# Kernel tuning notes

Measured on AMD Instinct MI355X. Metric: run time of the kernel, lower is better.

The kernel has to match this reference:

```python
import jax, jax.numpy as jnp
import numpy as np

GROUPS = 8
HEADS = 4
EPS = 1e-5


def setup_inputs() -> dict:
    key = jax.random.key(0)
    ks = jax.random.split(key, 5)
    b, c, h, w = 4, 256, 64, 64
    x = jax.random.normal(ks[0], (b, c, h, w), dtype=jnp.float32)
    gn_w = jnp.ones((c,), dtype=jnp.float32)
    gn_b = jnp.zeros((c,), dtype=jnp.float32)
    qkv_w = jax.random.normal(ks[1], (3 * c, c), dtype=jnp.float32) * (c ** -0.5)
    qkv_b = jax.random.normal(ks[2], (3 * c,), dtype=jnp.float32) * 0.01
    proj_w = jax.random.normal(ks[3], (c, c), dtype=jnp.float32) * (c ** -0.5)
    proj_b = jax.random.normal(ks[4], (c,), dtype=jnp.float32) * 0.01
    return {"x": x, "gn_w": gn_w, "gn_b": gn_b, "qkv_w": qkv_w,
            "qkv_b": qkv_b, "proj_w": proj_w, "proj_b": proj_b}


def reference(x, gn_w, gn_b, qkv_w, qkv_b, proj_w, proj_b):
    b, c, h, w = x.shape
    head_dim = c // HEADS
    n = h * w

    # GroupNorm (biased variance, per torch)
    xg = x.reshape(b, GROUPS, c // GROUPS, h, w)
    mean = xg.mean(axis=(2, 3, 4), keepdims=True)
    var = xg.var(axis=(2, 3, 4), keepdims=True)
    xn = ((xg - mean) * jax.lax.rsqrt(var + EPS)).reshape(b, c, h, w)
    xn = xn * gn_w[None, :, None, None] + gn_b[None, :, None, None]

    # 1x1 conv qkv: [b,3c,h,w]
    qkv = jnp.einsum('oc,bchw->bohw', qkv_w, xn) + qkv_b[None, :, None, None]
    # split channel dim as (3, heads, head_dim), flatten spatial -> [b,3,H,d,n]
    qkv = qkv.reshape(b, 3, HEADS, head_dim, n)
    q, k, v = qkv[:, 0], qkv[:, 1], qkv[:, 2]  # each [b,H,d,n]

    scale = head_dim ** -0.5
    attn = jnp.einsum('bhci,bhcj->bhij', q, k) * scale  # [b,H,n,n]
    attn = jax.nn.softmax(attn, axis=-1)
    out = jnp.einsum('bhij,bhcj->bhci', attn, v)  # [b,H,d,n]
    out = out.reshape(b, c, h, w)

    out = jnp.einsum('oc,bchw->bohw', proj_w, out) + proj_b[None, :, None, None]
    return out + x
```

## Files before the change

### kernel.cpp

```cpp
#include <hip/hip_runtime.h>
#include <math.h>

#define NPIX 4096
#define CCH 256

typedef __attribute__((ext_vector_type(4))) float f32x4;
typedef __attribute__((ext_vector_type(16))) float f32x16;
typedef __attribute__((ext_vector_type(8))) short s16x8;
typedef unsigned short u16;

__device__ __forceinline__ short bf16_rne(float x) {
  union { float f; unsigned u; } c; c.f = x;
  unsigned r = c.u + 0x7FFF + ((c.u >> 16) & 1);
  return (short)(r >> 16);
}
__device__ __forceinline__ unsigned cvtpk2(float lo, float hi) {
  unsigned r;
  asm("v_cvt_pk_bf16_f32 %0, %1, %2" : "=v"(r) : "v"(lo), "v"(hi));
  return r;
}
__device__ __forceinline__ unsigned pack2(float a, float b) {
  return cvtpk2(a, b);
}
__device__ __forceinline__ float max3f(float a, float b, float c) {
  float d;
  asm("v_max3_f32 %0, %1, %2, %3" : "=v"(d) : "v"(a), "v"(b), "v"(c));
  return d;
}
__device__ __forceinline__ float bf16_to_f32(unsigned short v) {
  return __uint_as_float(((unsigned)v) << 16);
}

__device__ __forceinline__ void plane32_swap(unsigned& a, unsigned& b) {
#if __has_builtin(__builtin_amdgcn_permlane32_swap)
  auto r = __builtin_amdgcn_permlane32_swap(a, b, false, false);
  a = r[0]; b = r[1];
#else
  asm("s_nop 2\n\tv_permlane32_swap_b32 %0, %1\n\ts_nop 2" : "+v"(a), "+v"(b));
#endif
}
__device__ __forceinline__ float red_max_half(float x) {
  unsigned a = __float_as_uint(x), b = a;
  plane32_swap(a, b);
  return fmaxf(__uint_as_float(a), __uint_as_float(b));
}
__device__ __forceinline__ float red_sum_half(float x) {
  unsigned a = __float_as_uint(x), b = a;
  plane32_swap(a, b);
  return __uint_as_float(a) + __uint_as_float(b);
}

#define QSCALE 0.18033688011f

__global__ __launch_bounds__(256) void gn_stats_wcvt(
    const float* __restrict__ x, const float* __restrict__ qkv_w, const float* __restrict__ proj_w,
    const float* __restrict__ qkv_b, double2* __restrict__ partials,
    u16* __restrict__ wq, u16* __restrict__ wp, float* __restrict__ biasq)
{
  const int blk = blockIdx.x, tid = threadIdx.x;
#pragma unroll
  for (int p = 0; p < 4; ++p) {
    int idx = blk * 1024 + p * 256 + tid;
    if (idx < 196608) {
      float v = qkv_w[idx];
      if (idx < 65536) v *= QSCALE;
      wq[idx] = (u16)bf16_rne(v);
    } else {
      int j = idx - 196608;
      wp[j] = (u16)bf16_rne(proj_w[j]);
    }
    if (idx < 768) {
      float bv = qkv_b[idx];
      if (idx < 256) bv *= QSCALE;
      biasq[idx] = bv;
    }
  }
  const int bg = blk >> 3, chunk = blk & 7;
  const float4* base = (const float4*)(x + (size_t)bg * 131072 + (size_t)chunk * 16384);
  double s = 0.0, ss = 0.0;
  for (int idx = tid; idx < 4096; idx += 256) {
    float4 v = base[idx];
    s  += (double)v.x + (double)v.y + (double)v.z + (double)v.w;
    ss += (double)v.x * v.x + (double)v.y * v.y + (double)v.z * v.z + (double)v.w * v.w;
  }
  __shared__ double rs[256], rss[256];
  rs[tid] = s; rss[tid] = ss;
  __syncthreads();
  for (int off = 128; off > 0; off >>= 1) {
    if (tid < off) { rs[tid] += rs[tid + off]; rss[tid] += rss[tid + off]; }
    __syncthreads();
  }
  if (tid == 0) {
    double2 p; p.x = rs[0]; p.y = rss[0];
    partials[blk] = p;
  }
}

__global__ __launch_bounds__(256) void gn_apply_t2(
    const float* __restrict__ x, const double2* __restrict__ partials,
    const float* __restrict__ gn_w, const float* __restrict__ gn_b,
    u16* __restrict__ Xt)
{
  const int b = blockIdx.z, c0 = blockIdx.y * 64, n0 = blockIdx.x * 64;
  const int tid = threadIdx.x;
  __shared__ u16 T[64 * 68];
  __shared__ float sal[64], sbe[64], smv[2], srv[2];
  if (tid < 2) {
    int bg = b * 8 + (c0 >> 5) + tid;
    double s = 0.0, ss = 0.0;
    for (int c = 0; c < 8; ++c) { double2 p = partials[bg * 8 + c]; s += p.x; ss += p.y; }
    double mean = s / 131072.0;
    double var  = ss / 131072.0 - mean * mean;
    smv[tid] = (float)mean;
    srv[tid] = (float)(1.0 / sqrt(var + 1e-5));
  }
  __syncthreads();
  if (tid < 64) {
    int g = tid >> 5;
    int ch = c0 + tid;
    float a = srv[g] * gn_w[ch];
    sal[tid] = a;
    sbe[tid] = gn_b[ch] - smv[g] * a;
  }
  __syncthreads();
  const int n4 = (tid & 15) * 4, cr = tid >> 4;
#pragma unroll
  for (int p = 0; p < 4; ++p) {
    int cl = cr + 16 * p;
    int c = c0 + cl;
    float a = sal[cl], bt = sbe[cl];
    float4 v = *(const float4*)&x[((size_t)b * CCH + c) * NPIX + n0 + n4];
    T[(n4 + 0) * 68 + cl] = (u16)bf16_rne(v.x * a + bt);
    T[(n4 + 1) * 68 + cl] = (u16)bf16_rne(v.y * a + bt);
    T[(n4 + 2) * 68 + cl] = (u16)bf16_rne(v.z * a + bt);
    T[(n4 + 3) * 68 + cl] = (u16)bf16_rne(v.w * a + bt);
  }
  __syncthreads();
#pragma unroll
  for (int it = 0; it < 2; ++it) {
    int linear = it * 256 + tid;
    int n = linear >> 3, ch = linear & 7;
    s16x8 v = *(const s16x8*)&T[n * 68 + ch * 8];
    *(s16x8*)&Xt[((size_t)b * NPIX + n0 + n) * CCH + c0 + ch * 8] = v;
  }
}

__global__ __launch_bounds__(256) void qkv_gemm_kernel(
    const u16* __restrict__ Wbf, const float* __restrict__ biasv, const u16* __restrict__ Xt,
    u16* __restrict__ Qt, u16* __restrict__ Kt, u16* __restrict__ Vb)
{
  const int nblk = blockIdx.x, m0 = blockIdx.y * 64;
  const int tid = threadIdx.x, wave = tid >> 6, lane = tid & 63;
  const int n16 = lane & 15, quad = lane >> 4;
  const int n0 = nblk * 128 + wave * 32;

  f32x4 acc[4][2];
#pragma unroll
  for (int a = 0; a < 4; ++a)
#pragma unroll
    for (int c = 0; c < 2; ++c) acc[a][c] = (f32x4){0.f, 0.f, 0.f, 0.f};

#pragma unroll
  for (int k0 = 0; k0 < 256; k0 += 32) {
    s16x8 af[4], bfr[2];
#pragma unroll
    for (int msub = 0; msub < 4; ++msub)
      af[msub] = *(const s16x8*)&Wbf[(size_t)(m0 + msub * 16 + n16) * 256 + k0 + quad * 8];
#pragma unroll
    for (int nsub = 0; nsub < 2; ++nsub)
      bfr[nsub] = *(const s16x8*)&Xt[(size_t)(n0 + nsub * 16 + n16) * 256 + k0 + quad * 8];
#pragma unroll
    for (int msub = 0; msub < 4; ++msub)
#pragma unroll
      for (int nsub = 0; nsub < 2; ++nsub)
        acc[msub][nsub] = __builtin_amdgcn_mfma_f32_16x16x32_bf16(af[msub], bfr[nsub], acc[msub][nsub], 0, 0, 0);
  }

  __shared__ u16 T[8704];
  if (m0 < 512) {
#pragma unroll
    for (int msub = 0; msub < 4; ++msub)
#pragma unroll
      for (int nsub = 0; nsub < 2; ++nsub) {
        float b0 = biasv[m0 + msub * 16 + quad * 4 + 0];
        float b1 = biasv[m0 + msub * 16 + quad * 4 + 1];
        float b2 = biasv[m0 + msub * 16 + quad * 4 + 2];
        float b3 = biasv[m0 + msub * 16 + quad * 4 + 3];
        uint2 w2;
        w2.x = pack2(acc[msub][nsub][0] + b0, acc[msub][nsub][1] + b1);
        w2.y = pack2(acc[msub][nsub][2] + b2, acc[msub][nsub][3] + b3);
        *(uint2*)&T[(wave * 32 + nsub * 16 + n16) * 68 + msub * 16 + quad * 4] = w2;
      }
    __syncthreads();
    u16* dst = (m0 < 256) ? Qt : Kt;
    const int coff = m0 & 255;
#pragma unroll
    for (int it = 0; it < 4; ++it) {
      int linear = it * 256 + tid;
      int n = linear >> 3, ch = linear & 7;
      s16x8 v = *(const s16x8*)&T[n * 68 + ch * 8];
      *(s16x8*)&dst[(size_t)(nblk * 128 + n) * 256 + coff + ch * 8] = v;
    }
  } else {
#pragma unroll
    for (int msub = 0; msub < 4; ++msub)
#pragma unroll
      for (int nsub = 0; nsub < 2; ++nsub) {
        int ncol = wave * 32 + nsub * 16 + n16;
#pragma unroll
        for (int r = 0; r < 4; ++r) {
          int m = msub * 16 + quad * 4 + r;
          T[m * 136 + ncol] = (u16)bf16_rne(acc[msub][nsub][r] + biasv[m0 + m]);
        }
      }
    __syncthreads();
    const int b = (nblk * 128) >> 12, i0n = (nblk * 128) & 4095;
#pragma unroll
    for (int it = 0; it < 4; ++it) {
      int linear = it * 256 + tid;
      int mloc = linear >> 4, ch = linear & 15;
      s16x8 v = *(const s16x8*)&T[mloc * 136 + ch * 8];
      int c = (m0 - 512) + mloc;
      *(s16x8*)&Vb[((size_t)b * CCH + c) * NPIX + i0n + ch * 8] = v;
    }
  }
}

__device__ __forceinline__ void kv_load6(
    const u16* __restrict__ Kb, const u16* __restrict__ Vg, int h, int j0, int sj, int part,
    s16x8& k0, s16x8& k1, s16x8& v0, s16x8& v1)
{
  const s16x8* kp = (const s16x8*)&Kb[(size_t)(j0 + sj) * 256 + h * 64 + part * 16];
  const s16x8* vp = (const s16x8*)&Vg[(size_t)sj * NPIX + j0 + part * 16];
  k0 = kp[0]; k1 = kp[1]; v0 = vp[0]; v1 = vp[1];
}
__device__ __forceinline__ void kv_store6(
    u16* Ksb, u16* Vsb, int sbase,
    s16x8 k0, s16x8 k1, s16x8 v0, s16x8 v1)
{
  *(s16x8*)&Ksb[sbase]       = k0;
  *(s16x8*)&Ksb[sbase + 256] = k1;
  *(s16x8*)&Vsb[sbase]       = v0;
  *(s16x8*)&Vsb[sbase + 256] = v1;
}

__device__ __forceinline__ void attn_tile6(
    const u16* Ksb, const u16* Vsb, const s16x8 qf[4], int lane,
    f32x16 ot[2], float& m_i, float& l_i)
{
  f32x16 st[2];
#pragma unroll
  for (int r = 0; r < 16; ++r) { st[0][r] = 0.f; st[1][r] = 0.f; }

  __builtin_amdgcn_s_setprio(1);
#pragma unroll
  for (int kq = 0; kq < 4; ++kq)
#pragma unroll
    for (int jsub = 0; jsub < 2; ++jsub) {
      s16x8 a = *(const s16x8*)&Ksb[(jsub * 4 + kq) * 512 + lane * 8];
      st[jsub] = __builtin_amdgcn_mfma_f32_32x32x16_bf16(a, qf[kq], st[jsub], 0, 0, 0);
    }
  __builtin_amdgcn_s_setprio(0);

  float c0 = max3f(st[0][0],  st[0][1],  st[0][2]);
  float c1 = max3f(st[0][3],  st[0][4],  st[0][5]);
  float c2 = max3f(st[0][6],  st[0][7],  st[0][8]);
  float c3 = max3f(st[0][9],  st[0][10], st[0][11]);
  float c4 = max3f(st[0][12], st[0][13], st[0][14]);
  float c5 = max3f(st[0][15], st[1][0],  st[1][1]);
  float c6 = max3f(st[1][2],  st[1][3],  st[1][4]);
  float c7 = max3f(st[1][5],  st[1][6],  st[1][7]);
  float c8 = max3f(st[1][8],  st[1][9],  st[1][10]);
  float c9 = max3f(st[1][11], st[1][12], st[1][13]);
  float d0 = max3f(c0, c1, c2);
  float d1 = max3f(c3, c4, c5);
  float d2 = max3f(c6, c7, c8);
  float d3 = max3f(c9, st[1][14], st[1][15]);
  float tm = fmaxf(fmaxf(d0, d1), fmaxf(d2, d3));
  tm = red_max_half(tm);

  if (__any(tm > m_i + 8.0f)) {
    float mn = fmaxf(m_i, tm);
    float al = __builtin_amdgcn_exp2f(m_i - mn);
    m_i = mn;
    l_i *= al;
#pragma unroll
    for (int r = 0; r < 16; ++r) { ot[0][r] *= al; ot[1][r] *= al; }
  }

#pragma unroll
  for (int f = 0; f < 2; ++f)
#pragma unroll
    for (int r = 0; r < 16; ++r)
      st[f][r] = __builtin_amdgcn_exp2f(st[f][r] - m_i);

  float s0 = (st[0][0] + st[0][1]) + (st[0][2]  + st[0][3]);
  float s1 = (st[0][4] + st[0][5]) + (st[0][6]  + st[0][7]);
  float s2 = (st[0][8] + st[0][9]) + (st[0][10] + st[0][11]);
  float s3 = (st[0][12]+ st[0][13])+ (st[0][14] + st[0][15]);
  float s4 = (st[1][0] + st[1][1]) + (st[1][2]  + st[1][3]);
  float s5 = (st[1][4] + st[1][5]) + (st[1][6]  + st[1][7]);
  float s6 = (st[1][8] + st[1][9]) + (st[1][10] + st[1][11]);
  float s7 = (st[1][12]+ st[1][13])+ (st[1][14] + st[1][15]);
  float ps = ((s0 + s1) + (s2 + s3)) + ((s4 + s5) + (s6 + s7));
  ps = red_sum_half(ps);
  l_i += ps;

#pragma unroll
  for (int jq = 0; jq < 4; ++jq) {
    const int jsub = jq >> 1;
    const int b0 = (jq & 1) * 8;
    const int b1 = b0 + 4;
    unsigned u0 = cvtpk2(st[jsub][b0 + 0], st[jsub][b0 + 1]);
    unsigned u1 = cvtpk2(st[jsub][b0 + 2], st[jsub][b0 + 3]);
    unsigned u2 = cvtpk2(st[jsub][b1 + 0], st[jsub][b1 + 1]);
    unsigned u3 = cvtpk2(st[jsub][b1 + 2], st[jsub][b1 + 3]);
    plane32_swap(u0, u2);
    plane32_swap(u1, u3);
    union { unsigned u[4]; s16x8 v; } pu;
    pu.u[0] = u0; pu.u[1] = u1; pu.u[2] = u2; pu.u[3] = u3;
    __builtin_amdgcn_s_setprio(1);
#pragma unroll
    for (int dsub = 0; dsub < 2; ++dsub) {
      s16x8 a = *(const s16x8*)&Vsb[(dsub * 4 + jq) * 512 + lane * 8];
      ot[dsub] = __builtin_amdgcn_mfma_f32_32x32x16_bf16(a, pu.v, ot[dsub], 0, 0, 0);
    }
    __builtin_amdgcn_s_setprio(0);
  }
}

__global__ __launch_bounds__(256, 4) void attn_kernel6(
    const u16* __restrict__ Qt, const u16* __restrict__ Kt,
    const u16* __restrict__ Vb, u16* __restrict__ P0, u16* __restrict__ P1,
    float* __restrict__ mlbuf)
{
  const int b = blockIdx.z, h = blockIdx.y;
  const int xb = blockIdx.x;
  const int half = xb >> 5, iblk = xb & 31;
  const int tid = threadIdx.x;
  const int wave = tid >> 6, lane = tid & 63;
  const int i0w = iblk * 128 + wave * 32;

  __shared__ u16 Ks[2][4096];
  __shared__ u16 Vs[2][4096];

  const u16* Qb = Qt + (size_t)b * NPIX * 256;
  const u16* Kb = Kt + (size_t)b * NPIX * 256;
  const u16* Vg = Vb + ((size_t)b * CCH + h * 64) * NPIX;

  s16x8 qf[4];
#pragma unroll
  for (int kq = 0; kq < 4; ++kq)
    qf[kq] = *(const s16x8*)&Qb[(size_t)(i0w + (lane & 31)) * 256 + h * 64 + kq * 16 + (lane >> 5) * 8];

  f32x16 ot[2];
#pragma unroll
  for (int r = 0; r < 16; ++r) { ot[0][r] = 0.f; ot[1][r] = 0.f; }
  float m_i = -1e30f;
  float l_i = 0.f;

  const int sj = tid >> 2;
  const int part = tid & 3;
  const int sbase = ((sj >> 5) * 4 + part) * 512 + (sj & 31) * 8;
  const int jbase = half * 2048;

  s16x8 k0, k1, v0, v1;

  kv_load6(Kb, Vg, h, jbase, sj, part, k0, k1, v0, v1);
  kv_store6(Ks[0], Vs[0], sbase, k0, k1, v0, v1);
  __syncthreads();

#pragma unroll 1
  for (int t = 0; t < 30; t += 2) {
    kv_load6(Kb, Vg, h, jbase + (t + 1) * 64, sj, part, k0, k1, v0, v1);
    attn_tile6(Ks[0], Vs[0], qf, lane, ot, m_i, l_i);
    kv_store6(Ks[1], Vs[1], sbase, k0, k1, v0, v1);
    __syncthreads();
    kv_load6(Kb, Vg, h, jbase + (t + 2) * 64, sj, part, k0, k1, v0, v1);
    attn_tile6(Ks[1], Vs[1], qf, lane, ot, m_i, l_i);
    kv_store6(Ks[0], Vs[0], sbase, k0, k1, v0, v1);
    __syncthreads();
  }
  kv_load6(Kb, Vg, h, jbase + 31 * 64, sj, part, k0, k1, v0, v1);
  attn_tile6(Ks[0], Vs[0], qf, lane, ot, m_i, l_i);
  kv_store6(Ks[1], Vs[1], sbase, k0, k1, v0, v1);
  __syncthreads();
  attn_tile6(Ks[1], Vs[1], qf, lane, ot, m_i, l_i);

  float rl = 1.0f / l_i;
  u16* dst = (half == 0) ? P0 : P1;
  const size_t rowbase = (size_t)((size_t)b * NPIX + i0w + (lane & 31)) * 256 + h * 64 + (lane >> 5) * 4;
#pragma unroll
  for (int dsub = 0; dsub < 2; ++dsub)
#pragma unroll
    for (int q = 0; q < 4; ++q) {
      uint2 w2;
      w2.x = cvtpk2(ot[dsub][4 * q + 0] * rl, ot[dsub][4 * q + 1] * rl);
      w2.y = cvtpk2(ot[dsub][4 * q + 2] * rl, ot[dsub][4 * q + 3] * rl);
      *(uint2*)&dst[rowbase + dsub * 32 + q * 8] = w2;
    }
  if (lane < 32) {
    int idx = half * 65536 + b * 16384 + h * 4096 + i0w + lane;
    float2 ml; ml.x = m_i; ml.y = l_i;
    *(float2*)&mlbuf[idx * 2] = ml;
  }
}

__global__ __launch_bounds__(256) void proj_gemm_cmb(
    const u16* __restrict__ Wp, const float* __restrict__ proj_b,
    const u16* __restrict__ P0, const u16* __restrict__ P1, const float* __restrict__ mlbuf,
    const float* __restrict__ x, float* __restrict__ out)
{
  const int nblk = blockIdx.x, m0 = blockIdx.y * 64;
  const int tid = threadIdx.x, wave = tid >> 6, lane = tid & 63;
  const int n16 = lane & 15, quad = lane >> 4;
  const int n0 = nblk * 128 + wave * 32;

  float w0h[2][4], w1h[2][4];
#pragma unroll
  for (int ns = 0; ns < 2; ++ns) {
    int row = n0 + ns * 16 + n16;
    int bb = row >> 12, ii = row & 4095;
#pragma unroll
    for (int h = 0; h < 4; ++h) {
      int idx = bb * 16384 + h * 4096 + ii;
      float2 ml0 = *(const float2*)&mlbuf[(size_t)idx * 2];
      float2 ml1 = *(const float2*)&mlbuf[(size_t)(65536 + idx) * 2];
      float m = fmaxf(ml0.x, ml1.x);
      float cc0 = ml0.y * __builtin_amdgcn_exp2f(ml0.x - m);
      float cc1 = ml1.y * __builtin_amdgcn_exp2f(ml1.x - m);
      float rn = 1.0f / (cc0 + cc1);
      w0h[ns][h] = cc0 * rn;
      w1h[ns][h] = cc1 * rn;
    }
  }

  f32x4 acc[4][2];
#pragma unroll
  for (int a = 0; a < 4; ++a)
#pragma unroll
    for (int c = 0; c < 2; ++c) acc[a][c] = (f32x4){0.f, 0.f, 0.f, 0.f};

#pragma unroll
  for (int k0 = 0; k0 < 256; k0 += 32) {
    const int h = k0 >> 6;
    s16x8 af[4], bfr[2];
#pragma unroll
    for (int msub = 0; msub < 4; ++msub)
      af[msub] = *(const s16x8*)&Wp[(size_t)(m0 + msub * 16 + n16) * 256 + k0 + quad * 8];
#pragma unroll
    for (int nsub = 0; nsub < 2; ++nsub) {
      int row = n0 + nsub * 16 + n16;
      size_t off = (size_t)row * 256 + k0 + quad * 8;
      s16x8 a = *(const s16x8*)&P0[off];
      s16x8 c = *(const s16x8*)&P1[off];
      float w0 = w0h[nsub][h], w1 = w1h[nsub][h];
      union { unsigned u[4]; s16x8 v; } o;
#pragma unroll
      for (int e = 0; e < 4; ++e) {
        float lo = w0 * bf16_to_f32((unsigned short)a[2 * e])     + w1 * bf16_to_f32((unsigned short)c[2 * e]);
        float hi = w0 * bf16_to_f32((unsigned short)a[2 * e + 1]) + w1 * bf16_to_f32((unsigned short)c[2 * e + 1]);
        o.u[e] = cvtpk2(lo, hi);
      }
      bfr[nsub] = o.v;
    }
#pragma unroll
    for (int msub = 0; msub < 4; ++msub)
#pragma unroll
      for (int nsub = 0; nsub < 2; ++nsub)
        acc[msub][nsub] = __builtin_amdgcn_mfma_f32_16x16x32_bf16(af[msub], bfr[nsub], acc[msub][nsub], 0, 0, 0);
  }

  __shared__ float T[64 * 132];
#pragma unroll
  for (int msub = 0; msub < 4; ++msub)
#pragma unroll
    for (int nsub = 0; nsub < 2; ++nsub) {
      int ncol = wave * 32 + nsub * 16 + n16;
#pragma unroll
      for (int r = 0; r < 4; ++r) {
        int m = msub * 16 + quad * 4 + r;
        T[m * 132 + ncol] = acc[msub][nsub][r];
      }
    }
  __syncthreads();
  const int b = (nblk * 128) >> 12, i0n = (nblk * 128) & 4095;
#pragma unroll
  for (int it = 0; it < 8; ++it) {
    int linear = it * 256 + tid;
    int m = linear >> 5, ch = linear & 31;
    f32x4 v = *(const f32x4*)&T[m * 132 + ch * 4];
    float bs = proj_b[m0 + m];
    size_t g = ((size_t)b * CCH + m0 + m) * NPIX + i0n + ch * 4;
    float4 rv = *(const float4*)&x[g];
    float4 o;
    o.x = v[0] + bs + rv.x; o.y = v[1] + bs + rv.y;
    o.z = v[2] + bs + rv.z; o.w = v[3] + bs + rv.w;
    *(float4*)&out[g] = o;
  }
}

extern "C" void kernel_launch(void* const* d_in, const int* in_sizes, int n_in,
                              void* d_out, int out_size, void* d_ws, size_t ws_size,
                              hipStream_t stream)
{
  const float* x      = (const float*)d_in[0];
  const float* gn_w   = (const float*)d_in[1];
  const float* gn_b   = (const float*)d_in[2];
  const float* qkv_w  = (const float*)d_in[3];
  const float* qkv_b  = (const float*)d_in[4];
  const float* proj_w = (const float*)d_in[5];
  const float* proj_b = (const float*)d_in[6];
  float* out = (float*)d_out;

  float* ws    = (float*)d_ws;
  float* biasq = ws + 2048;
  double2* partials = (double2*)(ws + 2816);
  u16*   wq    = (u16*)(ws + 4096);
  u16*   wp    = (u16*)(ws + 102400);
  u16*   Xt    = (u16*)(ws + 135168);
  u16*   Qt    = (u16*)(ws + 2232320);
  u16*   Kt    = (u16*)(ws + 4329472);
  u16*   Vb    = (u16*)(ws + 6426624);
  u16*   Ot    = (u16*)(ws + 8523776);
  float* mlbuf = ws + 10620928;

  u16* P0 = Xt;

  gn_stats_wcvt<<<256, 256, 0, stream>>>(x, qkv_w, proj_w, qkv_b, partials, wq, wp, biasq);
  gn_apply_t2<<<dim3(64, 4, 4), 256, 0, stream>>>(x, partials, gn_w, gn_b, Xt);
  qkv_gemm_kernel<<<dim3(128, 12), 256, 0, stream>>>(wq, biasq, Xt, Qt, Kt, Vb);
  attn_kernel6<<<dim3(64, 4, 4), 256, 0, stream>>>(Qt, Kt, Vb, P0, Ot, mlbuf);
  proj_gemm_cmb<<<dim3(128, 4), 256, 0, stream>>>(wp, proj_b, P0, Ot, mlbuf, x, out);
}
```

Baseline: 240.1 us.

## Load attention K/V fragments directly from global memory, removing LDS staging

The attention kernel no longer stages K and V tiles in double-buffered shared memory with block barriers. Each wave now reads its MFMA operand fragments for K and V directly from global memory into registers, once per 64-key tile. This removes the LDS writes, LDS reads and __syncthreads, but each of the four waves in a block now fetches the same K/V data separately. That raises L2/global traffic and exposes load latency without explicit prefetch.

```diff
diff --git a/kernel.cpp b/kernel.cpp
--- a/kernel.cpp
+++ b/kernel.cpp
@@ -226,28 +226,17 @@
   }
 }
 
-__device__ __forceinline__ void kv_load6(
-    const u16* __restrict__ Kb, const u16* __restrict__ Vg, int h, int j0, int sj, int part,
-    s16x8& k0, s16x8& k1, s16x8& v0, s16x8& v1)
-{
-  const s16x8* kp = (const s16x8*)&Kb[(size_t)(j0 + sj) * 256 + h * 64 + part * 16];
-  const s16x8* vp = (const s16x8*)&Vg[(size_t)sj * NPIX + j0 + part * 16];
-  k0 = kp[0]; k1 = kp[1]; v0 = vp[0]; v1 = vp[1];
-}
-__device__ __forceinline__ void kv_store6(
-    u16* Ksb, u16* Vsb, int sbase,
-    s16x8 k0, s16x8 k1, s16x8 v0, s16x8 v1)
-{
-  *(s16x8*)&Ksb[sbase]       = k0;
-  *(s16x8*)&Ksb[sbase + 256] = k1;
-  *(s16x8*)&Vsb[sbase]       = v0;
-  *(s16x8*)&Vsb[sbase + 256] = v1;
-}
-
-__device__ __forceinline__ void attn_tile6(
-    const u16* Ksb, const u16* Vsb, const s16x8 qf[4], int lane,
+__device__ __forceinline__ void attn_tile7(
+    const u16* kt, const u16* vt, const s16x8 qf[4],
     f32x16 ot[2], float& m_i, float& l_i)
 {
+  s16x8 kf[8];
+#pragma unroll
+  for (int jsub = 0; jsub < 2; ++jsub)
+#pragma unroll
+    for (int kq = 0; kq < 4; ++kq)
+      kf[jsub * 4 + kq] = *(const s16x8*)(kt + jsub * 32 * 256 + kq * 16);
+
   f32x16 st[2];
 #pragma unroll
   for (int r = 0; r < 16; ++r) { st[0][r] = 0.f; st[1][r] = 0.f; }
@@ -256,11 +245,16 @@
 #pragma unroll
   for (int kq = 0; kq < 4; ++kq)
 #pragma unroll
-    for (int jsub = 0; jsub < 2; ++jsub) {
-      s16x8 a = *(const s16x8*)&Ksb[(jsub * 4 + kq) * 512 + lane * 8];
-      st[jsub] = __builtin_amdgcn_mfma_f32_32x32x16_bf16(a, qf[kq], st[jsub], 0, 0, 0);
-    }
+    for (int jsub = 0; jsub < 2; ++jsub)
+      st[jsub] = __builtin_amdgcn_mfma_f32_32x32x16_bf16(kf[jsub * 4 + kq], qf[kq], st[jsub], 0, 0, 0);
   __builtin_amdgcn_s_setprio(0);
+
+  s16x8 vf[8];
+#pragma unroll
+  for (int dsub = 0; dsub < 2; ++dsub)
+#pragma unroll
+    for (int jq = 0; jq < 4; ++jq)
+      vf[dsub * 4 + jq] = *(const s16x8*)(vt + dsub * 32 * NPIX + jq * 16);
 
   float c0 = max3f(st[0][0],  st[0][1],  st[0][2]);
   float c1 = max3f(st[0][3],  st[0][4],  st[0][5]);
@@ -321,15 +315,13 @@
     pu.u[0] = u0; pu.u[1] = u1; pu.u[2] = u2; pu.u[3] = u3;
     __builtin_amdgcn_s_setprio(1);
 #pragma unroll
-    for (int dsub = 0; dsub < 2; ++dsub) {
-      s16x8 a = *(const s16x8*)&Vsb[(dsub * 4 + jq) * 512 + lane * 8];
-      ot[dsub] = __builtin_amdgcn_mfma_f32_32x32x16_bf16(a, pu.v, ot[dsub], 0, 0, 0);
-    }
+    for (int dsub = 0; dsub < 2; ++dsub)
+      ot[dsub] = __builtin_amdgcn_mfma_f32_32x32x16_bf16(vf[dsub * 4 + jq], pu.v, ot[dsub], 0, 0, 0);
     __builtin_amdgcn_s_setprio(0);
   }
 }
 
-__global__ __launch_bounds__(256, 4) void attn_kernel6(
+__global__ __launch_bounds__(256, 4) void attn_kernel7(
     const u16* __restrict__ Qt, const u16* __restrict__ Kt,
     const u16* __restrict__ Vb, u16* __restrict__ P0, u16* __restrict__ P1,
     float* __restrict__ mlbuf)
@@ -341,17 +333,16 @@
   const int wave = tid >> 6, lane = tid & 63;
   const int i0w = iblk * 128 + wave * 32;
 
-  __shared__ u16 Ks[2][4096];
-  __shared__ u16 Vs[2][4096];
-
   const u16* Qb = Qt + (size_t)b * NPIX * 256;
   const u16* Kb = Kt + (size_t)b * NPIX * 256;
   const u16* Vg = Vb + ((size_t)b * CCH + h * 64) * NPIX;
 
+  const int l31 = lane & 31, lh8 = (lane >> 5) * 8;
+
   s16x8 qf[4];
 #pragma unroll
   for (int kq = 0; kq < 4; ++kq)
-    qf[kq] = *(const s16x8*)&Qb[(size_t)(i0w + (lane & 31)) * 256 + h * 64 + kq * 16 + (lane >> 5) * 8];
+    qf[kq] = *(const s16x8*)&Qb[(size_t)(i0w + l31) * 256 + h * 64 + kq * 16 + lh8];
 
   f32x16 ot[2];
 #pragma unroll
@@ -359,37 +350,17 @@
   float m_i = -1e30f;
   float l_i = 0.f;
 
-  const int sj = tid >> 2;
-  const int part = tid & 3;
-  const int sbase = ((sj >> 5) * 4 + part) * 512 + (sj & 31) * 8;
-  const int jbase = half * 2048;
-
-  s16x8 k0, k1, v0, v1;
-
-  kv_load6(Kb, Vg, h, jbase, sj, part, k0, k1, v0, v1);
-  kv_store6(Ks[0], Vs[0], sbase, k0, k1, v0, v1);
-  __syncthreads();
+  const u16* kbase = Kb + (size_t)(half * 2048 + l31) * 256 + h * 64 + lh8;
+  const u16* vbase = Vg + (size_t)l31 * NPIX + half * 2048 + lh8;
 
 #pragma unroll 1
-  for (int t = 0; t < 30; t += 2) {
-    kv_load6(Kb, Vg, h, jbase + (t + 1) * 64, sj, part, k0, k1, v0, v1);
-    attn_tile6(Ks[0], Vs[0], qf, lane, ot, m_i, l_i);
-    kv_store6(Ks[1], Vs[1], sbase, k0, k1, v0, v1);
-    __syncthreads();
-    kv_load6(Kb, Vg, h, jbase + (t + 2) * 64, sj, part, k0, k1, v0, v1);
-    attn_tile6(Ks[1], Vs[1], qf, lane, ot, m_i, l_i);
-    kv_store6(Ks[0], Vs[0], sbase, k0, k1, v0, v1);
-    __syncthreads();
-  }
-  kv_load6(Kb, Vg, h, jbase + 31 * 64, sj, part, k0, k1, v0, v1);
-  attn_tile6(Ks[0], Vs[0], qf, lane, ot, m_i, l_i);
-  kv_store6(Ks[1], Vs[1], sbase, k0, k1, v0, v1);
-  __syncthreads();
-  attn_tile6(Ks[1], Vs[1], qf, lane, ot, m_i, l_i);
+  for (int t = 0; t < 32; ++t) {
+    attn_tile7(kbase + (size_t)t * 64 * 256, vbase + t * 64, qf, ot, m_i, l_i);
+  }
 
   float rl = 1.0f / l_i;
   u16* dst = (half == 0) ? P0 : P1;
-  const size_t rowbase = (size_t)((size_t)b * NPIX + i0w + (lane & 31)) * 256 + h * 64 + (lane >> 5) * 4;
+  const size_t rowbase = (size_t)((size_t)b * NPIX + i0w + l31) * 256 + h * 64 + (lane >> 5) * 4;
 #pragma unroll
   for (int dsub = 0; dsub < 2; ++dsub)
 #pragma unroll
@@ -530,6 +501,6 @@
   gn_stats_wcvt<<<256, 256, 0, stream>>>(x, qkv_w, proj_w, qkv_b, partials, wq, wp, biasq);
   gn_apply_t2<<<dim3(64, 4, 4), 256, 0, stream>>>(x, partials, gn_w, gn_b, Xt);
   qkv_gemm_kernel<<<dim3(128, 12), 256, 0, stream>>>(wq, biasq, Xt, Qt, Kt, Vb);
-  attn_kernel6<<<dim3(64, 4, 4), 256, 0, stream>>>(Qt, Kt, Vb, P0, Ot, mlbuf);
+  attn_kernel7<<<dim3(64, 4, 4), 256, 0, stream>>>(Qt, Kt, Vb, P0, Ot, mlbuf);
   proj_gemm_cmb<<<dim3(128, 4), 256, 0, stream>>>(wp, proj_b, P0, Ot, mlbuf, x, out);
 }
```

Result: slower. 407.9 us (+69.9%).
